# Kernel tuning notes

Measured on AMD Instinct MI355X. Metric: run time of the kernel, lower is better.

## Reference

```python
import jax, jax.numpy as jnp
import numpy as np

B, N, H, HEADS = 8, 1024, 512, 4  # batch graphs, nodes/graph, graph_hsz, attention heads
R = 64  # relations per graph (passthrough)


def setup_inputs() -> dict:
    key = jax.random.key(0)
    k1, k2, k3, k4, k5, k6, k7 = jax.random.split(key, 7)
    adjs = jax.random.randint(k1, (B, N, N), 0, 2, dtype=jnp.int32)  # 0 => masked
    nodes = jax.random.normal(k2, (B, N, H), dtype=jnp.float32)
    triples = jax.random.normal(k3, (B, R, H), dtype=jnp.float32)   # unused in gat path
    relations = jax.random.normal(k4, (B, R, H), dtype=jnp.float32)  # passthrough
    node_num = jnp.full((B,), N, dtype=jnp.int32)  # all graphs full => no padding branch
    s = 1.0 / np.sqrt(H)
    Wq = (jax.random.normal(k5, (H, H), dtype=jnp.float32) * s)
    Wk = (jax.random.normal(k6, (H, H), dtype=jnp.float32) * s)
    Wv = (jax.random.normal(k7, (H, H), dtype=jnp.float32) * s)
    return {"adjs": adjs, "triples": triples, "nodes": nodes, "node_num": node_num,
            "relations": relations, "Wq": Wq, "Wk": Wk, "Wv": Wv}


def reference(adjs, triples, nodes, node_num, relations, Wq, Wk, Wv):
    b, n, h = nodes.shape
    dk = h // HEADS
    scale = 1.0 / jnp.sqrt(jnp.float32(h))  # torch divides by sqrt(key_dim)=sqrt(H)

    def to_heads(x, W):  # [B,N,H] -> [B,heads,N,dk]; matches split(dim=-1)+stack
        return (x @ W).reshape(b, n, HEADS, dk).transpose(0, 2, 1, 3)

    Q = to_heads(nodes, Wq)
    K = to_heads(nodes, Wk)
    V = to_heads(nodes, Wv)
    att = jnp.einsum('bhnd,bhmd->bhnm', Q, K) * scale
    att = jnp.where((adjs == 0)[:, None, :, :], -jnp.inf, att)
    p = jax.nn.softmax(att, axis=-1)  # dropout_p = blockdrop = 0.0 => identity
    out = jnp.einsum('bhnm,bhmd->bhnd', p, V)
    out = out.transpose(0, 2, 1, 3).reshape(b, n, h)  # concat heads along feature dim
    out = jax.nn.relu(out)
    return (out, relations)
```

## Files before the change

### kernel.cpp

```cpp
#include <hip/hip_runtime.h>
#include <stdint.h>

typedef __attribute__((ext_vector_type(4))) float f32x4;
typedef __attribute__((ext_vector_type(16))) float f32x16;
typedef __attribute__((ext_vector_type(8))) short bf16x8;
typedef unsigned long long ull;

#define GLB_AS const __attribute__((address_space(1)))
#define LDS_AS __attribute__((address_space(3)))

__device__ __forceinline__ short f2bf(float f) {
    union { float f; unsigned u; } x; x.f = f;
    unsigned r = x.u + 0x7FFFu + ((x.u >> 16) & 1u);
    return (short)(r >> 16);
}

__global__ void k_pre(const float* __restrict__ nodes, short* __restrict__ nodes_bf,
                      const float* __restrict__ Wq, const float* __restrict__ Wk,
                      const float* __restrict__ Wv, short* __restrict__ WT,
                      const int* __restrict__ adjs, unsigned* __restrict__ packed) {
    int bi = blockIdx.x, tid = threadIdx.x;
    if (bi < 2048) {
        int i = (bi * 256 + tid) * 8;
        float4 a = *(const float4*)(nodes + i);
        float4 b = *(const float4*)(nodes + i + 4);
        bf16x8 v;
        v[0] = f2bf(a.x); v[1] = f2bf(a.y); v[2] = f2bf(a.z); v[3] = f2bf(a.w);
        v[4] = f2bf(b.x); v[5] = f2bf(b.y); v[6] = f2bf(b.z); v[7] = f2bf(b.w);
        *(bf16x8*)(nodes_bf + i) = v;
    } else if (bi < 5120) {
        int g = (bi - 2048) * 256 + tid;
        int j = g >> 9, k = g & 511;
        int w = j >> 9, n = j & 511;
        const float* W = (w == 0) ? Wq : (w == 1) ? Wk : Wv;
        WT[g] = f2bf(W[k * 512 + n]);
    } else {
        int g = (bi - 5120) * 256 + tid;
        int wv = g >> 6, lane = g & 63;
        ull m = __ballot(adjs[(size_t)wv * 64 + lane] != 0);
        if (lane == 0) *(ull*)(packed + (size_t)wv * 2) = m;
    }
}

__global__ __launch_bounds__(256) void k_gemm_qkv(const short* __restrict__ A,
                                                  const short* __restrict__ WT,
                                                  short* __restrict__ C) {
    __shared__ short Asm[2][128 * 32];
    __shared__ short Bsm[2][128 * 32];
    const int tid = threadIdx.x;
    const int l = tid & 63, w = tid >> 6;
    const int wr = w >> 1, wc = w & 1;
    const int c16 = l & 15, g = l >> 4;
    const int wg = blockIdx.x;
    const int swz = (wg & 7) * 96 + (wg >> 3);
    const int row0 = (swz / 12) * 128, n0 = (swz % 12) * 128;
    f32x4 acc[4][4] = {};

    auto stage = [&](int kt, int bsel) {
        const int k0 = kt * 32;
#pragma unroll
        for (int i = 0; i < 2; ++i) {
            int ch = tid + 256 * i;
            int r = ch >> 2, gc = ch & 3;
            __builtin_amdgcn_global_load_lds((GLB_AS unsigned*)(A + (row0 + r) * 512 + k0 + 8 * gc),
                                             (LDS_AS unsigned*)(&Asm[bsel][ch * 8]), 16, 0, 0);
            __builtin_amdgcn_global_load_lds((GLB_AS unsigned*)(WT + (n0 + r) * 512 + k0 + 8 * gc),
                                             (LDS_AS unsigned*)(&Bsm[bsel][ch * 8]), 16, 0, 0);
        }
    };

    stage(0, 0);
    asm volatile("s_waitcnt vmcnt(0)" ::: "memory");
    __syncthreads();

    for (int kt = 0; kt < 16; ++kt) {
        const int cur = kt & 1;
        if (kt < 15) stage(kt + 1, cur ^ 1);
        bf16x8 af[4], bfr[4];
#pragma unroll
        for (int mf = 0; mf < 4; ++mf)
            af[mf] = *(const bf16x8*)&Asm[cur][(wr * 64 + mf * 16 + c16) * 32 + 8 * g];
#pragma unroll
        for (int nf = 0; nf < 4; ++nf)
            bfr[nf] = *(const bf16x8*)&Bsm[cur][(wc * 64 + nf * 16 + c16) * 32 + 8 * g];
#pragma unroll
        for (int mf = 0; mf < 4; ++mf)
#pragma unroll
            for (int nf = 0; nf < 4; ++nf)
                acc[mf][nf] = __builtin_amdgcn_mfma_f32_16x16x32_bf16(af[mf], bfr[nf], acc[mf][nf], 0, 0, 0);
        asm volatile("s_waitcnt vmcnt(0)" ::: "memory");
        __syncthreads();
    }
#pragma unroll
    for (int mf = 0; mf < 4; ++mf)
#pragma unroll
        for (int nf = 0; nf < 4; ++nf) {
            const float cs = (n0 + wc * 64 + nf * 16 < 512) ? 0.06375872022286384f : 1.0f;
#pragma unroll
            for (int r = 0; r < 4; ++r) {
                int row = row0 + wr * 64 + mf * 16 + 4 * g + r;
                int col = n0 + wc * 64 + nf * 16 + c16;
                C[row * 1536 + col] = f2bf(acc[mf][nf][r] * cs);
            }
        }
}

__global__ __launch_bounds__(256) void k_mid(const short* __restrict__ QKV, short* __restrict__ Vt2,
                                             short* __restrict__ Kt2,
                                             const float* __restrict__ rel_in, float* __restrict__ rel_out) {
    const int bi = blockIdx.x, t = threadIdx.x;
    if (bi >= 1280) {
        int g = (bi - 1280) * 256 + t;
        int c = g & 63, m = (g >> 6) & 1023, b = g >> 16;
        int h = c >> 4, khc = c & 15;
        bf16x8 v = *(const bf16x8*)(QKV + (size_t)(b * 1024 + m) * 1536 + 512 + c * 8);
        *(bf16x8*)(Kt2 + ((((size_t)(b * 4 + h) * 32 + (m >> 5)) * 16 + khc) * 32 + (m & 31)) * 8) = v;
        return;
    }
    if (bi >= 1024) {
        int i = ((bi - 1024) * 256 + t) * 4;
        *(float4*)(rel_out + i) = *(const float4*)(rel_in + i);
        return;
    }
    __shared__ short tile[64 * 65];
    const int b = bi >> 7, n0 = ((bi >> 3) & 15) * 64, d0 = (bi & 7) * 64;
#pragma unroll
    for (int i = 0; i < 16; ++i) {
        int idx = t + 256 * i;
        int nn = idx >> 6, dd = idx & 63;
        tile[nn * 65 + dd] = QKV[(b * 1024 + n0 + nn) * 1536 + 1024 + d0 + dd];
    }
    __syncthreads();
#pragma unroll
    for (int i = 0; i < 2; ++i) {
        int c = t + 256 * i;
        int dd = c >> 3, nl = (c & 7) * 8;
        int dg = d0 + dd;
        int h = dg >> 7, dh = dg & 127;
        bf16x8 v;
#pragma unroll
        for (int e = 0; e < 8; ++e)
            v[e] = tile[(nl + e) * 65 + dd];
        *(bf16x8*)(Vt2 + ((((size_t)(b * 4 + h)) * 128 + ((n0 + nl) >> 3)) * 128 + dh) * 8) = v;
    }
}

__global__ __launch_bounds__(512, 2) void k_attn(const short* __restrict__ QKV, const short* __restrict__ Kt2,
                                                 const short* __restrict__ Vt2,
                                                 const unsigned* __restrict__ packed, float* __restrict__ out) {
    __shared__ char smem[66560];
    float* Osh = (float*)smem;
    float* lsh = (float*)(smem + 65536);
    const int bh = blockIdx.x;
    const int b = bh >> 2, h = bh & 3;
    const int q0 = blockIdx.y * 128;
    const int tid = threadIdx.x, l = tid & 63, wid = tid >> 6;
    const int mg = wid >> 2, wq = wid & 3;
    const int l31 = l & 31, hi = l >> 5;
    const int qw = q0 + wq * 32;

    bf16x8 aq[8];
    const short* Qb = QKV + (size_t)(b * 1024 + qw + l31) * 1536 + h * 128;
#pragma unroll
    for (int kk = 0; kk < 8; ++kk)
        aq[kk] = *(const bf16x8*)(Qb + kk * 16 + hi * 8);

    f32x16 acc[4] = {};
    float l_lane = 0.f;

    const short* K2b = Kt2 + (size_t)(b * 4 + h) * 131072;
    const short* V2b = Vt2 + (size_t)(b * 4 + h) * 131072;
    const unsigned* adjw = packed + (size_t)(b * 1024 + qw + l31) * 32 + mg * 16;

    bf16x8 kcur[8], knxt[8], vcur[8];
    {
        const int mt = mg * 16;
#pragma unroll
        for (int kk = 0; kk < 8; ++kk)
            kcur[kk] = *(const bf16x8*)(K2b + ((size_t)(mt * 16 + 2 * kk + hi) * 32 + l31) * 8);
    }
    unsigned mcur = adjw[0];

#pragma unroll
    for (int t = 0; t < 16; ++t) {
        const int mc0 = mg * 64 + t * 4;
#pragma unroll
        for (int ks = 0; ks < 2; ++ks)
#pragma unroll
            for (int dd = 0; dd < 4; ++dd)
                vcur[ks * 4 + dd] = *(const bf16x8*)(V2b + ((size_t)(mc0 + 2 * ks + hi) * 128 + dd * 32 + l31) * 8);
        unsigned mnx = 0;
        if (t < 15) {
            const int mt = mg * 16 + t + 1;
#pragma unroll
            for (int kk = 0; kk < 8; ++kk)
                knxt[kk] = *(const bf16x8*)(K2b + ((size_t)(mt * 16 + 2 * kk + hi) * 32 + l31) * 8);
            mnx = adjw[t + 1];
        }

        f32x16 s = (f32x16)0.f;
        __builtin_amdgcn_s_setprio(1);
#pragma unroll
        for (int kk = 0; kk < 8; ++kk)
            s = __builtin_amdgcn_mfma_f32_32x32x16_bf16(kcur[kk], aq[kk], s, 0, 0, 0);
        __builtin_amdgcn_s_setprio(0);

        unsigned pk[4][2];
        const unsigned mshift = mcur >> (4 * hi);
        float lt = 0.f;
#pragma unroll
        for (int j = 0; j < 4; ++j) {
            float p[4];
#pragma unroll
            for (int r = 0; r < 4; ++r) {
                float e = __builtin_amdgcn_exp2f(s[4 * j + r]);
                p[r] = ((mshift >> (8 * j + r)) & 1u) ? e : 0.f;
            }
            lt += (p[0] + p[1]) + (p[2] + p[3]);
            asm("v_cvt_pk_bf16_f32 %0, %1, %2" : "=v"(pk[j][0]) : "v"(p[0]), "v"(p[1]));
            asm("v_cvt_pk_bf16_f32 %0, %1, %2" : "=v"(pk[j][1]) : "v"(p[2]), "v"(p[3]));
        }
        l_lane += lt;

        union fragu { unsigned u[4]; bf16x8 v; };
        fragu frag[2];
#pragma unroll
        for (int kh = 0; kh < 2; ++kh) {
            unsigned a0 = pk[2 * kh][0], a1 = pk[2 * kh][1];
            unsigned b0 = pk[2 * kh + 1][0], b1 = pk[2 * kh + 1][1];
            unsigned rx0 = (unsigned)__shfl_xor((int)a0, 32);
            unsigned rx1 = (unsigned)__shfl_xor((int)a1, 32);
            unsigned rx2 = (unsigned)__shfl_xor((int)b0, 32);
            unsigned rx3 = (unsigned)__shfl_xor((int)b1, 32);
            fragu f;
            f.u[0] = hi ? rx2 : a0;
            f.u[1] = hi ? rx3 : a1;
            f.u[2] = hi ? b0 : rx0;
            f.u[3] = hi ? b1 : rx1;
            frag[kh] = f;
        }

        __builtin_amdgcn_s_setprio(1);
#pragma unroll
        for (int ks = 0; ks < 2; ++ks)
#pragma unroll
            for (int dd = 0; dd < 4; ++dd)
                acc[dd] = __builtin_amdgcn_mfma_f32_32x32x16_bf16(frag[ks].v, vcur[ks * 4 + dd], acc[dd], 0, 0, 0);
        __builtin_amdgcn_s_setprio(0);

#pragma unroll
        for (int kk = 0; kk < 8; ++kk) kcur[kk] = knxt[kk];
        mcur = mnx;
    }

    l_lane += __shfl_xor(l_lane, 32);
    if (hi == 0) lsh[mg * 128 + wq * 32 + l31] = l_lane;

    if (mg == 1) {
#pragma unroll
        for (int dd = 0; dd < 4; ++dd)
#pragma unroll
            for (int j = 0; j < 4; ++j)
#pragma unroll
                for (int r = 0; r < 4; ++r) {
                    int qrow = wq * 32 + r + 8 * j + 4 * hi;
                    Osh[qrow * 128 + dd * 32 + l31] = acc[dd][4 * j + r];
                }
    }
    __syncthreads();
    if (mg == 0) {
        float invq[16];
#pragma unroll
        for (int j = 0; j < 4; ++j)
#pragma unroll
            for (int r = 0; r < 4; ++r) {
                int qrow = wq * 32 + r + 8 * j + 4 * hi;
                invq[4 * j + r] = 1.f / (lsh[qrow] + lsh[128 + qrow]);
            }
#pragma unroll
        for (int dd = 0; dd < 4; ++dd)
#pragma unroll
            for (int j = 0; j < 4; ++j)
#pragma unroll
                for (int r = 0; r < 4; ++r) {
                    int qrow = wq * 32 + r + 8 * j + 4 * hi;
                    float o = (acc[dd][4 * j + r] + Osh[qrow * 128 + dd * 32 + l31]) * invq[4 * j + r];
                    out[(size_t)(b * 1024 + q0 + qrow) * 512 + h * 128 + dd * 32 + l31] = fmaxf(o, 0.f);
                }
    }
}

extern "C" void kernel_launch(void* const* d_in, const int* in_sizes, int n_in,
                              void* d_out, int out_size, void* d_ws, size_t ws_size,
                              hipStream_t stream) {
    const int*   adjs      = (const int*)d_in[0];
    const float* nodes     = (const float*)d_in[2];
    const float* relations = (const float*)d_in[4];
    const float* Wq        = (const float*)d_in[5];
    const float* Wk        = (const float*)d_in[6];
    const float* Wv        = (const float*)d_in[7];

    char* ws = (char*)d_ws;
    short* nodes_bf   = (short*)(ws);
    short* WT         = (short*)(ws + 8388608);
    short* QKV        = (short*)(ws + 9961472);
    short* Vt2        = (short*)(ws + 35127296);
    unsigned* adjpack = (unsigned*)(ws + 43515904);
    short* Kt2        = (short*)(ws + 44564480);

    float* out     = (float*)d_out;
    float* out_rel = out + 4194304;

    k_pre<<<dim3(37888), dim3(256), 0, stream>>>(nodes, nodes_bf, Wq, Wk, Wv, WT, adjs, adjpack);
    k_gemm_qkv<<<dim3(768), dim3(256), 0, stream>>>(nodes_bf, WT, QKV);
    k_mid<<<dim3(3328), dim3(256), 0, stream>>>(QKV, Vt2, Kt2, relations, out_rel);
    k_attn<<<dim3(32, 8), dim3(512), 0, stream>>>(QKV, Kt2, Vt2, adjpack, out);
}
```

Before: 80.03 us.

## Split attention keys four ways with smaller query tiles and tree reduction

```diff
diff --git a/kernel.cpp b/kernel.cpp
--- a/kernel.cpp
+++ b/kernel.cpp
@@ -145,17 +145,18 @@
     }
 }
 
-__global__ __launch_bounds__(512, 2) void k_attn(const short* __restrict__ QKV, const short* __restrict__ Kt2,
+__global__ __launch_bounds__(512, 4) void k_attn(const short* __restrict__ QKV, const short* __restrict__ Kt2,
                                                  const short* __restrict__ Vt2,
                                                  const unsigned* __restrict__ packed, float* __restrict__ out) {
     __shared__ char smem[66560];
-    float* Osh = (float*)smem;
-    float* lsh = (float*)(smem + 65536);
+    float* OshA = (float*)smem;
+    float* OshB = (float*)(smem + 32768);
+    float* lsh  = (float*)(smem + 65536);
     const int bh = blockIdx.x;
     const int b = bh >> 2, h = bh & 3;
-    const int q0 = blockIdx.y * 128;
+    const int q0 = blockIdx.y * 64;
     const int tid = threadIdx.x, l = tid & 63, wid = tid >> 6;
-    const int mg = wid >> 2, wq = wid & 3;
+    const int mg = wid >> 1, wq = wid & 1;
     const int l31 = l & 31, hi = l >> 5;
     const int qw = q0 + wq * 32;
 
@@ -170,11 +171,11 @@
 
     const short* K2b = Kt2 + (size_t)(b * 4 + h) * 131072;
     const short* V2b = Vt2 + (size_t)(b * 4 + h) * 131072;
-    const unsigned* adjw = packed + (size_t)(b * 1024 + qw + l31) * 32 + mg * 16;
+    const unsigned* adjw = packed + (size_t)(b * 1024 + qw + l31) * 32 + mg * 8;
 
     bf16x8 kcur[8], knxt[8], vcur[8];
     {
-        const int mt = mg * 16;
+        const int mt = mg * 8;
 #pragma unroll
         for (int kk = 0; kk < 8; ++kk)
             kcur[kk] = *(const bf16x8*)(K2b + ((size_t)(mt * 16 + 2 * kk + hi) * 32 + l31) * 8);
@@ -182,16 +183,16 @@
     unsigned mcur = adjw[0];
 
 #pragma unroll
-    for (int t = 0; t < 16; ++t) {
-        const int mc0 = mg * 64 + t * 4;
+    for (int t = 0; t < 8; ++t) {
+        const int mc0 = mg * 32 + t * 4;
 #pragma unroll
         for (int ks = 0; ks < 2; ++ks)
 #pragma unroll
             for (int dd = 0; dd < 4; ++dd)
                 vcur[ks * 4 + dd] = *(const bf16x8*)(V2b + ((size_t)(mc0 + 2 * ks + hi) * 128 + dd * 32 + l31) * 8);
         unsigned mnx = 0;
-        if (t < 15) {
-            const int mt = mg * 16 + t + 1;
+        if (t < 7) {
+            const int mt = mg * 8 + t + 1;
 #pragma unroll
             for (int kk = 0; kk < 8; ++kk)
                 knxt[kk] = *(const bf16x8*)(K2b + ((size_t)(mt * 16 + 2 * kk + hi) * 32 + l31) * 8);
@@ -254,9 +255,10 @@
     }
 
     l_lane += __shfl_xor(l_lane, 32);
-    if (hi == 0) lsh[mg * 128 + wq * 32 + l31] = l_lane;
-
-    if (mg == 1) {
+    if (hi == 0) lsh[mg * 64 + wq * 32 + l31] = l_lane;
+
+    if (mg == 1 || mg == 3) {
+        float* O = (mg == 1) ? OshA : OshB;
 #pragma unroll
         for (int dd = 0; dd < 4; ++dd)
 #pragma unroll
@@ -264,7 +266,32 @@
 #pragma unroll
                 for (int r = 0; r < 4; ++r) {
                     int qrow = wq * 32 + r + 8 * j + 4 * hi;
-                    Osh[qrow * 128 + dd * 32 + l31] = acc[dd][4 * j + r];
+                    O[qrow * 128 + dd * 32 + l31] = acc[dd][4 * j + r];
+                }
+    }
+    __syncthreads();
+    if (mg == 0 || mg == 2) {
+        const float* O = (mg == 0) ? OshA : OshB;
+#pragma unroll
+        for (int dd = 0; dd < 4; ++dd)
+#pragma unroll
+            for (int j = 0; j < 4; ++j)
+#pragma unroll
+                for (int r = 0; r < 4; ++r) {
+                    int qrow = wq * 32 + r + 8 * j + 4 * hi;
+                    acc[dd][4 * j + r] += O[qrow * 128 + dd * 32 + l31];
+                }
+    }
+    __syncthreads();
+    if (mg == 2) {
+#pragma unroll
+        for (int dd = 0; dd < 4; ++dd)
+#pragma unroll
+            for (int j = 0; j < 4; ++j)
+#pragma unroll
+                for (int r = 0; r < 4; ++r) {
+                    int qrow = wq * 32 + r + 8 * j + 4 * hi;
+                    OshA[qrow * 128 + dd * 32 + l31] = acc[dd][4 * j + r];
                 }
     }
     __syncthreads();
@@ -275,7 +302,7 @@
 #pragma unroll
             for (int r = 0; r < 4; ++r) {
                 int qrow = wq * 32 + r + 8 * j + 4 * hi;
-                invq[4 * j + r] = 1.f / (lsh[qrow] + lsh[128 + qrow]);
+                invq[4 * j + r] = 1.f / (lsh[qrow] + lsh[64 + qrow] + lsh[128 + qrow] + lsh[192 + qrow]);
             }
 #pragma unroll
         for (int dd = 0; dd < 4; ++dd)
@@ -284,7 +311,7 @@
 #pragma unroll
                 for (int r = 0; r < 4; ++r) {
                     int qrow = wq * 32 + r + 8 * j + 4 * hi;
-                    float o = (acc[dd][4 * j + r] + Osh[qrow * 128 + dd * 32 + l31]) * invq[4 * j + r];
+                    float o = (acc[dd][4 * j + r] + OshA[qrow * 128 + dd * 32 + l31]) * invq[4 * j + r];
                     out[(size_t)(b * 1024 + q0 + qrow) * 512 + h * 128 + dd * 32 + l31] = fmaxf(o, 0.f);
                 }
     }
@@ -314,5 +341,5 @@
     k_pre<<<dim3(37888), dim3(256), 0, stream>>>(nodes, nodes_bf, Wq, Wk, Wv, WT, adjs, adjpack);
     k_gemm_qkv<<<dim3(768), dim3(256), 0, stream>>>(nodes_bf, WT, QKV);
     k_mid<<<dim3(3328), dim3(256), 0, stream>>>(QKV, Vt2, Kt2, relations, out_rel);
-    k_attn<<<dim3(32, 8), dim3(512), 0, stream>>>(QKV, Kt2, Vt2, adjpack, out);
-}
+    k_attn<<<dim3(32, 16), dim3(512), 0, stream>>>(QKV, Kt2, Vt2, adjpack, out);
+}
```

After: 277.4 us. 3.47x slower.

## Fuse K/V relayout into QKV GEMM epilogue and drop the middle kernel

Applied to the files above, without the earlier changes.

```diff
diff --git a/kernel.cpp b/kernel.cpp
--- a/kernel.cpp
+++ b/kernel.cpp
@@ -4,6 +4,7 @@
 typedef __attribute__((ext_vector_type(4))) float f32x4;
 typedef __attribute__((ext_vector_type(16))) float f32x16;
 typedef __attribute__((ext_vector_type(8))) short bf16x8;
+typedef __attribute__((ext_vector_type(4))) short short4v;
 typedef unsigned long long ull;
 
 #define GLB_AS const __attribute__((address_space(1)))
@@ -18,7 +19,7 @@
 __global__ void k_pre(const float* __restrict__ nodes, short* __restrict__ nodes_bf,
                       const float* __restrict__ Wq, const float* __restrict__ Wk,
                       const float* __restrict__ Wv, short* __restrict__ WT,
-                      const int* __restrict__ adjs, unsigned* __restrict__ packed) {
+                      const float* __restrict__ rel_in, float* __restrict__ rel_out) {
     int bi = blockIdx.x, tid = threadIdx.x;
     if (bi < 2048) {
         int i = (bi * 256 + tid) * 8;
@@ -35,24 +36,32 @@
         const float* W = (w == 0) ? Wq : (w == 1) ? Wk : Wv;
         WT[g] = f2bf(W[k * 512 + n]);
     } else {
-        int g = (bi - 5120) * 256 + tid;
+        int i = ((bi - 5120) * 256 + tid) * 4;
+        *(float4*)(rel_out + i) = *(const float4*)(rel_in + i);
+    }
+}
+
+__global__ __launch_bounds__(256) void k_gemm_pack(const short* __restrict__ A,
+                                                   const short* __restrict__ WT,
+                                                   short* __restrict__ Qbuf,
+                                                   short* __restrict__ Kt2,
+                                                   short* __restrict__ Vt2,
+                                                   const int* __restrict__ adjs,
+                                                   unsigned* __restrict__ packed) {
+    const int bi = blockIdx.x, tid = threadIdx.x;
+    if (bi >= 768) {
+        int g = (bi - 768) * 256 + tid;
         int wv = g >> 6, lane = g & 63;
         ull m = __ballot(adjs[(size_t)wv * 64 + lane] != 0);
         if (lane == 0) *(ull*)(packed + (size_t)wv * 2) = m;
-    }
-}
-
-__global__ __launch_bounds__(256) void k_gemm_qkv(const short* __restrict__ A,
-                                                  const short* __restrict__ WT,
-                                                  short* __restrict__ C) {
+        return;
+    }
     __shared__ short Asm[2][128 * 32];
     __shared__ short Bsm[2][128 * 32];
-    const int tid = threadIdx.x;
     const int l = tid & 63, w = tid >> 6;
     const int wr = w >> 1, wc = w & 1;
     const int c16 = l & 15, g = l >> 4;
-    const int wg = blockIdx.x;
-    const int swz = (wg & 7) * 96 + (wg >> 3);
+    const int swz = (bi & 7) * 96 + (bi >> 3);
     const int row0 = (swz / 12) * 128, n0 = (swz % 12) * 128;
     f32x4 acc[4][4] = {};
 
@@ -91,61 +100,42 @@
         asm volatile("s_waitcnt vmcnt(0)" ::: "memory");
         __syncthreads();
     }
+
+    const int bb = row0 >> 10;
+    const int nbase0 = row0 & 1023;
 #pragma unroll
     for (int mf = 0; mf < 4; ++mf)
 #pragma unroll
         for (int nf = 0; nf < 4; ++nf) {
-            const float cs = (n0 + wc * 64 + nf * 16 < 512) ? 0.06375872022286384f : 1.0f;
-#pragma unroll
-            for (int r = 0; r < 4; ++r) {
-                int row = row0 + wr * 64 + mf * 16 + 4 * g + r;
-                int col = n0 + wc * 64 + nf * 16 + c16;
-                C[row * 1536 + col] = f2bf(acc[mf][nf][r] * cs);
+            const int colb = n0 + wc * 64 + nf * 16;
+            const int col = colb + c16;
+            const int rowb = row0 + wr * 64 + mf * 16 + 4 * g;
+            if (colb < 512) {
+#pragma unroll
+                for (int r = 0; r < 4; ++r)
+                    Qbuf[(size_t)(rowb + r) * 512 + col] = f2bf(acc[mf][nf][r] * 0.06375872022286384f);
+            } else if (colb < 1024) {
+                const int kg = col - 512;
+                const int hh = kg >> 7, kh = kg & 127;
+                const int mb = (rowb & 1023);
+                short* base = Kt2 + (((size_t)(bb * 4 + hh) * 16 + (kh >> 3)) * 1024) * 8 + (kh & 7);
+#pragma unroll
+                for (int r = 0; r < 4; ++r)
+                    base[(size_t)(mb + r) * 8] = f2bf(acc[mf][nf][r]);
+            } else {
+                const int dg = col - 1024;
+                const int hh = dg >> 7, dh = dg & 127;
+                const int nb8 = (nbase0 + wr * 64 + mf * 16 + 4 * g) >> 3;
+                const int off = (g & 1) * 4;
+                short4v v;
+                v[0] = f2bf(acc[mf][nf][0]); v[1] = f2bf(acc[mf][nf][1]);
+                v[2] = f2bf(acc[mf][nf][2]); v[3] = f2bf(acc[mf][nf][3]);
+                *(short4v*)(Vt2 + (((size_t)(bb * 4 + hh) * 128 + nb8) * 128 + dh) * 8 + off) = v;
             }
         }
 }
 
-__global__ __launch_bounds__(256) void k_mid(const short* __restrict__ QKV, short* __restrict__ Vt2,
-                                             short* __restrict__ Kt2,
-                                             const float* __restrict__ rel_in, float* __restrict__ rel_out) {
-    const int bi = blockIdx.x, t = threadIdx.x;
-    if (bi >= 1280) {
-        int g = (bi - 1280) * 256 + t;
-        int c = g & 63, m = (g >> 6) & 1023, b = g >> 16;
-        int h = c >> 4, khc = c & 15;
-        bf16x8 v = *(const bf16x8*)(QKV + (size_t)(b * 1024 + m) * 1536 + 512 + c * 8);
-        *(bf16x8*)(Kt2 + ((((size_t)(b * 4 + h) * 32 + (m >> 5)) * 16 + khc) * 32 + (m & 31)) * 8) = v;
-        return;
-    }
-    if (bi >= 1024) {
-        int i = ((bi - 1024) * 256 + t) * 4;
-        *(float4*)(rel_out + i) = *(const float4*)(rel_in + i);
-        return;
-    }
-    __shared__ short tile[64 * 65];
-    const int b = bi >> 7, n0 = ((bi >> 3) & 15) * 64, d0 = (bi & 7) * 64;
-#pragma unroll
-    for (int i = 0; i < 16; ++i) {
-        int idx = t + 256 * i;
-        int nn = idx >> 6, dd = idx & 63;
-        tile[nn * 65 + dd] = QKV[(b * 1024 + n0 + nn) * 1536 + 1024 + d0 + dd];
-    }
-    __syncthreads();
-#pragma unroll
-    for (int i = 0; i < 2; ++i) {
-        int c = t + 256 * i;
-        int dd = c >> 3, nl = (c & 7) * 8;
-        int dg = d0 + dd;
-        int h = dg >> 7, dh = dg & 127;
-        bf16x8 v;
-#pragma unroll
-        for (int e = 0; e < 8; ++e)
-            v[e] = tile[(nl + e) * 65 + dd];
-        *(bf16x8*)(Vt2 + ((((size_t)(b * 4 + h)) * 128 + ((n0 + nl) >> 3)) * 128 + dh) * 8) = v;
-    }
-}
-
-__global__ __launch_bounds__(512, 2) void k_attn(const short* __restrict__ QKV, const short* __restrict__ Kt2,
+__global__ __launch_bounds__(512, 2) void k_attn(const short* __restrict__ Qbuf, const short* __restrict__ Kt2,
                                                  const short* __restrict__ Vt2,
                                                  const unsigned* __restrict__ packed, float* __restrict__ out) {
     __shared__ char smem[66560];
@@ -160,7 +150,7 @@
     const int qw = q0 + wq * 32;
 
     bf16x8 aq[8];
-    const short* Qb = QKV + (size_t)(b * 1024 + qw + l31) * 1536 + h * 128;
+    const short* Qb = Qbuf + (size_t)(b * 1024 + qw + l31) * 512 + h * 128;
 #pragma unroll
     for (int kk = 0; kk < 8; ++kk)
         aq[kk] = *(const bf16x8*)(Qb + kk * 16 + hi * 8);
@@ -177,7 +167,7 @@
         const int mt = mg * 16;
 #pragma unroll
         for (int kk = 0; kk < 8; ++kk)
-            kcur[kk] = *(const bf16x8*)(K2b + ((size_t)(mt * 16 + 2 * kk + hi) * 32 + l31) * 8);
+            kcur[kk] = *(const bf16x8*)(K2b + ((size_t)(2 * kk + hi) * 1024 + mt * 32 + l31) * 8);
     }
     unsigned mcur = adjw[0];
 
@@ -194,7 +184,7 @@
             const int mt = mg * 16 + t + 1;
 #pragma unroll
             for (int kk = 0; kk < 8; ++kk)
-                knxt[kk] = *(const bf16x8*)(K2b + ((size_t)(mt * 16 + 2 * kk + hi) * 32 + l31) * 8);
+                knxt[kk] = *(const bf16x8*)(K2b + ((size_t)(2 * kk + hi) * 1024 + mt * 32 + l31) * 8);
             mnx = adjw[t + 1];
         }
 
@@ -303,16 +293,15 @@
     char* ws = (char*)d_ws;
     short* nodes_bf   = (short*)(ws);
     short* WT         = (short*)(ws + 8388608);
-    short* QKV        = (short*)(ws + 9961472);
-    short* Vt2        = (short*)(ws + 35127296);
-    unsigned* adjpack = (unsigned*)(ws + 43515904);
-    short* Kt2        = (short*)(ws + 44564480);
+    short* Qbuf       = (short*)(ws + 9961472);
+    short* Vt2        = (short*)(ws + 18350080);
+    short* Kt2        = (short*)(ws + 26738688);
+    unsigned* adjpack = (unsigned*)(ws + 35127296);
 
     float* out     = (float*)d_out;
     float* out_rel = out + 4194304;
 
-    k_pre<<<dim3(37888), dim3(256), 0, stream>>>(nodes, nodes_bf, Wq, Wk, Wv, WT, adjs, adjpack);
-    k_gemm_qkv<<<dim3(768), dim3(256), 0, stream>>>(nodes_bf, WT, QKV);
-    k_mid<<<dim3(3328), dim3(256), 0, stream>>>(QKV, Vt2, Kt2, relations, out_rel);
-    k_attn<<<dim3(32, 8), dim3(512), 0, stream>>>(QKV, Kt2, Vt2, adjpack, out);
-}
+    k_pre<<<dim3(5376), dim3(256), 0, stream>>>(nodes, nodes_bf, Wq, Wk, Wv, WT, relations, out_rel);
+    k_gemm_pack<<<dim3(33536), dim3(256), 0, stream>>>(nodes_bf, WT, Qbuf, Kt2, Vt2, adjs, adjpack);
+    k_attn<<<dim3(32, 8), dim3(512), 0, stream>>>(Qbuf, Kt2, Vt2, adjpack, out);
+}
```

Result: slower. 86.22 us (+7.7%).
